# Kernel optimization log

Measured on AMD Instinct MI355X. Metric: run time of the kernel, lower is better.

Reference implementation:

```python
import jax, jax.numpy as jnp
import numpy as np

HID = 768
NUM_HEADS = 12
HEAD_DIM = HID // NUM_HEADS
MASK_VALUE = -1.0e9
EPS = 1.0e-4  # module's self.eps, also used as the diagonal fill constant


def setup_inputs() -> dict:
    key = jax.random.key(0)
    k1, k2, k3 = jax.random.split(key, 3)
    B, M = 16, 512
    ocr_features = jax.random.normal(k1, (B, M, HID), dtype=jnp.float32)
    # prior neighbor-attention from previous layer, probabilities in [0,1)
    prior = jax.random.uniform(k2, (B, 1, M, M), dtype=jnp.float32)
    Wq = jax.random.normal(k3, (HID, HID), dtype=jnp.float32) / np.sqrt(HID)
    bq = jnp.zeros((HID,), dtype=jnp.float32)
    ocr_features_mask = jnp.ones((B, M), dtype=jnp.int32)
    return {"ocr_features": ocr_features, "prior": prior, "Wq": Wq, "bq": bq,
            "ocr_features_mask": ocr_features_mask}


def reference(ocr_features, prior, Wq, bq, ocr_features_mask):
    B, M, _ = ocr_features.shape
    # Module uses q_linear for Q, K (and V, which is unused) -> Q == K.
    q = (ocr_features @ Wq + bq).reshape(B, M, NUM_HEADS, HEAD_DIM)
    q = q.transpose(0, 2, 1, 3)  # (B, H, M, D)
    # note: scaled by head_dim (not sqrt), as in the source
    scores = jnp.einsum('bhid,bhjd->bhij', q, q) / HEAD_DIM  # (B, H, M, M)

    dt = scores.dtype
    prev_word_mask = jnp.eye(M, k=1, dtype=dt)   # superdiagonal
    next_word_mask = jnp.eye(M, k=-1, dtype=dt)  # subdiagonal
    main_diag_mask = jnp.eye(M, dtype=dt)

    # neighbor mask: only prev/next word positions that are valid OCR tokens
    neibor_mask = ((prev_word_mask + next_word_mask)[None, :, :] > 0) & \
                  (ocr_features_mask[:, None, :] > 0)  # (B, M, M)
    scores = jnp.where(neibor_mask[:, None, :, :], scores, MASK_VALUE)
    neibor_attn = jax.nn.softmax(scores, axis=-1)
    # symmetrize: sqrt(a * a^T + eps)
    neibor_attn = jnp.sqrt(neibor_attn * jnp.swapaxes(neibor_attn, -1, -2) + EPS)
    neibor_attn = prior + (1.0 - prior) * neibor_attn

    # log-space cumulative product via triangular matmuls
    tri = jnp.triu(jnp.ones((M, M), dtype=dt))  # (M, M), incl. diagonal
    # keep only superdiagonal log-probs, cumulative-sum to the right via tri
    t = jnp.where(prev_word_mask > 0, jnp.log(neibor_attn + 1e-9), 0.0) @ tri
    g_attn = jnp.exp(jnp.einsum('ij,bhjk->bhik', tri, t))
    # zero out diagonal and lower triangle (tri - diag == 0 there)
    g_attn = jnp.where((tri - main_diag_mask) > 0, g_attn, 0.0)
    g_attn = g_attn + jnp.swapaxes(g_attn, -1, -2) + \
             jnp.where(main_diag_mask > 0, neibor_attn, EPS)
    return (g_attn, neibor_attn)
```

## Files before the change

kernel.cpp:

```cpp
#include <hip/hip_runtime.h>
#include <cstdint>
#include <cstddef>

#define B_   16
#define M_   512
#define HID_ 768
#define NH_  12
#define HD_  64

typedef short s16x8 __attribute__((ext_vector_type(8)));
typedef float f32x4 __attribute__((ext_vector_type(4)));
typedef unsigned short u16x8 __attribute__((ext_vector_type(8)));
typedef unsigned short u16x4 __attribute__((ext_vector_type(4)));

__device__ __forceinline__ unsigned short f2bf(float f) {
    unsigned int u = __builtin_bit_cast(unsigned int, f);
    u = u + 0x7FFFu + ((u >> 16) & 1u);
    return (unsigned short)(u >> 16);
}

__device__ __forceinline__ void gld_lds16(const void* g, void* lds) {
    __builtin_amdgcn_global_load_lds(
        (const __attribute__((address_space(1))) unsigned int*)g,
        (__attribute__((address_space(3))) unsigned int*)lds,
        16, 0, 0);
}

__device__ __forceinline__ int csx(int r, int c) {
    return (r << 7) | (c ^ (r & 31));
}

__launch_bounds__(256)
__global__ void prep(const float* __restrict__ X, const float* __restrict__ W,
                     unsigned short* __restrict__ Xb, unsigned short* __restrict__ Wt) {
    __shared__ float T[32][33];
    const int blk = blockIdx.x;
    const int t   = threadIdx.x;
    if (blk < 3072) {
        const size_t i = ((size_t)blk * 256 + t) * 8;
        const float4 a = *(const float4*)(X + i);
        const float4 b = *(const float4*)(X + i + 4);
        u16x8 v = { f2bf(a.x), f2bf(a.y), f2bf(a.z), f2bf(a.w),
                    f2bf(b.x), f2bf(b.y), f2bf(b.z), f2bf(b.w) };
        *(u16x8*)(Xb + i) = v;
    } else {
        const int tb = blk - 3072;
        const int n0 = (tb % 24) * 32;
        const int k0 = (tb / 24) * 32;
        #pragma unroll
        for (int p = 0; p < 4; ++p) {
            const int r = p * 8 + (t >> 5);
            const int c = t & 31;
            T[r][c] = W[(size_t)(k0 + r) * HID_ + n0 + c];
        }
        __syncthreads();
        const int nl = t >> 3;
        const int k4 = (t & 7) * 4;
        u16x4 v = { f2bf(T[k4 + 0][nl]), f2bf(T[k4 + 1][nl]),
                    f2bf(T[k4 + 2][nl]), f2bf(T[k4 + 3][nl]) };
        *(u16x4*)(Wt + (size_t)(n0 + nl) * HID_ + k0 + k4) = v;
    }
}

__launch_bounds__(256)
__global__ void gemm_dots(const unsigned short* __restrict__ Xb,
                          const unsigned short* __restrict__ Wt,
                          const float* __restrict__ bq,
                          float* __restrict__ sdot, float* __restrict__ Qedge) {
    __shared__ float smem[64 * 128];
    __shared__ float partial[128];
    unsigned short* As = (unsigned short*)smem;
    unsigned short* Bs = (unsigned short*)smem + 64 * 64;
    float* Cs = smem;

    const int tid  = threadIdx.x;
    const int lane = tid & 63;
    const int wave = tid >> 6;
    const int wr   = (wave >> 1) * 32;
    const int wc   = (wave & 1) * 64;
    const int ln   = lane & 15;
    const int quad = lane >> 4;

    const int bid = blockIdx.x;
    const int li  = bid >> 3;
    const int by  = ((bid & 7) << 4) + li / 6;
    const int bx  = li % 6;
    const int r0  = by * 64;
    const int n0  = bx * 128;

    const int srow  = lane >> 3;
    const int selem = ((lane & 7) ^ (lane >> 3)) * 8;
    const int swz   = (ln & 7) << 4;

    f32x4 acc[2][4] = {};

    for (int kt = 0; kt < HID_ / 64; ++kt) {
        const int k0 = kt * 64;
        #pragma unroll
        for (int c = wave * 2; c < wave * 2 + 2; ++c) {
            const unsigned short* ga = Xb + (size_t)(r0 + c * 8 + srow) * HID_ + k0 + selem;
            gld_lds16(ga, (char*)As + c * 1024);
        }
        #pragma unroll
        for (int c = wave * 4; c < wave * 4 + 4; ++c) {
            const unsigned short* gb = Wt + (size_t)(n0 + c * 8 + srow) * HID_ + k0 + selem;
            gld_lds16(gb, (char*)Bs + c * 1024);
        }
        __syncthreads();

        #pragma unroll
        for (int kk = 0; kk < 2; ++kk) {
            s16x8 af[2], bf[4];
            #pragma unroll
            for (int r = 0; r < 2; ++r)
                af[r] = *(const s16x8*)((const char*)As + (wr + r * 16 + ln) * 128
                                        + ((kk * 64 + quad * 16) ^ swz));
            #pragma unroll
            for (int c = 0; c < 4; ++c)
                bf[c] = *(const s16x8*)((const char*)Bs + (wc + c * 16 + ln) * 128
                                        + ((kk * 64 + quad * 16) ^ swz));
            #pragma unroll
            for (int r = 0; r < 2; ++r)
                #pragma unroll
                for (int c = 0; c < 4; ++c)
                    acc[r][c] = __builtin_amdgcn_mfma_f32_16x16x32_bf16(af[r], bf[c], acc[r][c], 0, 0, 0);
        }
        __syncthreads();
    }

    #pragma unroll
    for (int c = 0; c < 4; ++c) {
        const int col = wc + c * 16 + ln;
        const float bias = bq[n0 + col];
        #pragma unroll
        for (int r = 0; r < 2; ++r) {
            const int rowb = wr + r * 16 + quad * 4;
            #pragma unroll
            for (int e = 0; e < 4; ++e)
                Cs[csx(rowb + e, col)] = acc[r][c][e] + bias;
        }
    }
    __syncthreads();

    {
        const int s   = tid >> 7;
        const int col = tid & 127;
        const int row = s ? 63 : 0;
        Qedge[(size_t)(by * 2 + s) * HID_ + n0 + col] = Cs[csx(row, col)];
    }

    {
        const int p  = tid & 63;
        const int hh = (tid >> 6) & 1;
        const int dh = tid >> 7;
        float s0 = 0.f, s1 = 0.f;
        if (p < 63) {
            const int base = hh * 64 + dh * 32;
            #pragma unroll
            for (int d = 0; d < 32; d += 2) {
                s0 += Cs[csx(p, base + d)]     * Cs[csx(p + 1, base + d)];
                s1 += Cs[csx(p, base + d + 1)] * Cs[csx(p + 1, base + d + 1)];
            }
        }
        if (dh) partial[(hh << 6) | p] = s0 + s1;
        __syncthreads();
        if (!dh && p < 63) {
            const float tot = s0 + s1 + partial[(hh << 6) | p];
            const int g  = by * 64 + p;
            const int bb = g >> 9;
            const int ii = g & 511;
            const int h  = bx * 2 + hh;
            sdot[(size_t)(bb * NH_ + h) * M_ + ii] = tot * (1.f / 64.f);
        }
    }
}

__launch_bounds__(512)
__global__ void scanstats(const float* __restrict__ sdot, const float* __restrict__ Qedge,
                          const float* __restrict__ prior, const int* __restrict__ mask,
                          float* __restrict__ na_super, float* __restrict__ na_sub,
                          float* __restrict__ Ssum) {
    const int bh = blockIdx.x;
    const int b  = bh / NH_;
    const int h  = bh - b * NH_;
    const int i  = threadIdx.x;
    const int lane = i & 63;
    const int wid  = i >> 6;

    __shared__ float sh_s[M_];
    __shared__ float sh_pp[M_];
    __shared__ float wsum[8];

    float s = 0.f;
    if (i < M_ - 1) {
        if ((i & 63) == 63) {
            const int gby = (b << 3) + (i >> 6);
            const float* qa = Qedge + (size_t)(gby * 2 + 1) * HID_ + h * HD_;
            const float* qb = Qedge + (size_t)(gby + 1) * 2 * HID_ + h * HD_;
            float a0 = 0.f, a1 = 0.f;
            #pragma unroll
            for (int d = 0; d < HD_; d += 8) {
                const float4 xa = *(const float4*)(qa + d);
                const float4 xb = *(const float4*)(qb + d);
                const float4 ya = *(const float4*)(qa + d + 4);
                const float4 yb = *(const float4*)(qb + d + 4);
                a0 += xa.x * xb.x + xa.y * xb.y + xa.z * xb.z + xa.w * xb.w;
                a1 += ya.x * yb.x + ya.y * yb.y + ya.z * yb.z + ya.w * yb.w;
            }
            s = (a0 + a1) * (1.f / 64.f);
        } else {
            s = sdot[bh * M_ + i];
        }
    }
    sh_s[i] = s;
    __syncthreads();

    const bool vp = (i > 0)      && (mask[b * M_ + i - 1] > 0);
    const bool vn = (i < M_ - 1) && (mask[b * M_ + i + 1] > 0);
    const float sp = vp ? sh_s[i - 1] : -1e30f;
    const float sn = vn ? s : -1e30f;
    const float mx = fmaxf(sp, sn);
    const float ep = vp ? __expf(sp - mx) : 0.f;
    const float en = vn ? __expf(sn - mx) : 0.f;
    float den = ep + en;
    den = (den > 0.f) ? den : 1.f;
    const float pp = ep / den;
    const float pn = en / den;
    sh_pp[i] = pp;
    __syncthreads();

    float Lv = 0.f;
    if (i < M_ - 1) {
        const float  sym = sqrtf(pn * sh_pp[i + 1] + 1e-4f);
        const size_t pb  = (size_t)b * (M_ * M_);
        const float  prs = prior[pb + (size_t)i * M_ + (i + 1)];
        const float  prb = prior[pb + (size_t)(i + 1) * M_ + i];
        const float  nsup = prs + (1.f - prs) * sym;
        na_super[bh * M_ + i] = nsup;
        na_sub[bh * M_ + i]   = prb + (1.f - prb) * sym;
        Lv = logf(nsup + 1e-9f);
    }

    float v = Lv;
    #pragma unroll
    for (int off = 1; off < 64; off <<= 1) {
        float tt = __shfl_up(v, off, 64);
        if (lane >= off) v += tt;
    }
    if (lane == 63) wsum[wid] = v;
    __syncthreads();
    float base = 0.f;
    for (int w = 0; w < wid; ++w) base += wsum[w];
    Ssum[bh * M_ + i] = v + base - Lv;
}

__launch_bounds__(256)
__global__ void fill_out(const float* __restrict__ prior,
                         const float* __restrict__ na_super,
                         const float* __restrict__ na_sub,
                         const float* __restrict__ Ssum,
                         float* __restrict__ out) {
    const int tid = threadIdx.x;
    const int bi  = blockIdx.x;
    const int b   = bi >> 8;
    const int i   = ((bi & 255) << 1) | (tid >> 7);
    const int j0  = (tid & 127) * 4;

    const f32x4 pr4 = __builtin_nontemporal_load(
        (const f32x4*)(prior + (size_t)b * (M_ * M_) + (size_t)i * M_ + j0));
    const float pv[4] = {pr4[0], pr4[1], pr4[2], pr4[3]};
    const float c0 = 0.00999999977f;
    const size_t half = (size_t)B_ * NH_ * M_ * M_;

    #pragma unroll 2
    for (int h = 0; h < NH_; ++h) {
        const int bh = b * NH_ + h;
        const float4 S4 = *(const float4*)(Ssum + (size_t)bh * M_ + j0);
        const float  Si = Ssum[bh * M_ + i];
        const float  nsup_i   = (i < M_ - 1) ? na_super[bh * M_ + i]   : 0.f;
        const float  nsub_im1 = (i > 0)      ? na_sub[bh * M_ + i - 1] : 0.f;
        const float sv[4] = {S4.x, S4.y, S4.z, S4.w};

        f32x4 nav, ggv;
        #pragma unroll
        for (int e = 0; e < 4; ++e) {
            const int j = j0 + e;
            float na = fmaf(pv[e], 1.f - c0, c0);
            if (j == i - 1) na = nsub_im1;
            if (j == i + 1) na = nsup_i;
            const float d = sv[e] - Si;
            float g = __expf((j > i) ? d : -d) + 1e-4f;
            if (j == i) g = na;
            nav[e] = na;
            ggv[e] = g;
        }

        const size_t off = ((size_t)(bh * M_ + i)) * M_ + j0;
        __builtin_nontemporal_store(ggv, (f32x4*)(out + off));
        __builtin_nontemporal_store(nav, (f32x4*)(out + half + off));
    }
}

extern "C" void kernel_launch(void* const* d_in, const int* in_sizes, int n_in,
                              void* d_out, int out_size, void* d_ws, size_t ws_size,
                              hipStream_t stream) {
    const float* X     = (const float*)d_in[0];
    const float* prior = (const float*)d_in[1];
    const float* Wq    = (const float*)d_in[2];
    const float* bq    = (const float*)d_in[3];
    const int*   msk   = (const int*)  d_in[4];
    float* out = (float*)d_out;

    float* na_super = (float*)d_ws;
    float* na_sub   = na_super + (size_t)B_ * NH_ * M_;
    float* Ssum     = na_sub   + (size_t)B_ * NH_ * M_;
    float* sdot     = Ssum     + (size_t)B_ * NH_ * M_;
    float* Qedge    = sdot     + (size_t)B_ * NH_ * M_;
    unsigned short* Xb = (unsigned short*)(Qedge + (size_t)128 * 2 * HID_);
    unsigned short* Wt = Xb + (size_t)B_ * M_ * HID_;

    prep<<<3072 + 576, 256, 0, stream>>>(X, Wq, Xb, Wt);

    gemm_dots<<<768, 256, 0, stream>>>(Xb, Wt, bq, sdot, Qedge);

    scanstats<<<B_ * NH_, M_, 0, stream>>>(sdot, Qedge, prior, msk, na_super, na_sub, Ssum);

    fill_out<<<B_ * (M_ / 2), 256, 0, stream>>>(prior, na_super, na_sub, Ssum, out);
}
```

Baseline: 453.7 us.

## Move bulk neighbor-attention output writes into GEMM kernel to overlap with MFMA

The bulk of the neighbor-attention output (prior*(1-c0)+c0 for every head) is now written from inside the GEMM kernel's k-loop, spread across iterations, so those memory stores overlap with matrix compute. The scan kernel scatters the sub- and superdiagonal values straight into the output, and fill_out writes only the g_attn half plus the diagonal. This removes the na_super/na_sub workspace and halves the store traffic in the last kernel. In exchange the GEMM gains extra global traffic that may compete with its tile loads, and correctness now depends on the order of the three kernels' writes.

```diff
diff --git a/kernel.cpp b/kernel.cpp
--- a/kernel.cpp
+++ b/kernel.cpp
@@ -12,6 +12,8 @@
 typedef float f32x4 __attribute__((ext_vector_type(4)));
 typedef unsigned short u16x8 __attribute__((ext_vector_type(8)));
 typedef unsigned short u16x4 __attribute__((ext_vector_type(4)));
+
+#define C0_ 0.00999999977f
 
 __device__ __forceinline__ unsigned short f2bf(float f) {
     unsigned int u = __builtin_bit_cast(unsigned int, f);
@@ -66,7 +68,9 @@
 __global__ void gemm_dots(const unsigned short* __restrict__ Xb,
                           const unsigned short* __restrict__ Wt,
                           const float* __restrict__ bq,
-                          float* __restrict__ sdot, float* __restrict__ Qedge) {
+                          const float* __restrict__ prior,
+                          float* __restrict__ sdot, float* __restrict__ Qedge,
+                          float* __restrict__ out) {
     __shared__ float smem[64 * 128];
     __shared__ float partial[128];
     unsigned short* As = (unsigned short*)smem;
@@ -92,6 +96,9 @@
     const int selem = ((lane & 7) ^ (lane >> 3)) * 8;
     const int swz   = (ln & 7) << 4;
 
+    const size_t half  = (size_t)B_ * NH_ * M_ * M_;
+    const int    fbase = bid * 65536 + tid * 4;
+
     f32x4 acc[2][4] = {};
 
     for (int kt = 0; kt < HID_ / 64; ++kt) {
@@ -107,6 +114,24 @@
             gld_lds16(gb, (char*)Bs + c * 1024);
         }
         __syncthreads();
+
+        {
+            const int qb = kt * 6;
+            #pragma unroll
+            for (int qq = 0; qq < 6; ++qq) {
+                const int q = qb + qq;
+                if (q < 64) {
+                    const int f   = fbase + (q << 10);
+                    const int bh  = f >> 18;
+                    const int bb2 = bh / NH_;
+                    const int rem = f & 0x3FFFF;
+                    const float4 p4 = *(const float4*)(prior + ((size_t)bb2 << 18) + rem);
+                    f32x4 na4 = { fmaf(p4.x, 1.f - C0_, C0_), fmaf(p4.y, 1.f - C0_, C0_),
+                                  fmaf(p4.z, 1.f - C0_, C0_), fmaf(p4.w, 1.f - C0_, C0_) };
+                    __builtin_nontemporal_store(na4, (f32x4*)(out + half + f));
+                }
+            }
+        }
 
         #pragma unroll
         for (int kk = 0; kk < 2; ++kk) {
@@ -178,8 +203,7 @@
 __launch_bounds__(512)
 __global__ void scanstats(const float* __restrict__ sdot, const float* __restrict__ Qedge,
                           const float* __restrict__ prior, const int* __restrict__ mask,
-                          float* __restrict__ na_super, float* __restrict__ na_sub,
-                          float* __restrict__ Ssum) {
+                          float* __restrict__ Ssum, float* __restrict__ out) {
     const int bh = blockIdx.x;
     const int b  = bh / NH_;
     const int h  = bh - b * NH_;
@@ -236,9 +260,12 @@
         const float  prs = prior[pb + (size_t)i * M_ + (i + 1)];
         const float  prb = prior[pb + (size_t)(i + 1) * M_ + i];
         const float  nsup = prs + (1.f - prs) * sym;
-        na_super[bh * M_ + i] = nsup;
-        na_sub[bh * M_ + i]   = prb + (1.f - prb) * sym;
+        const float  nsub = prb + (1.f - prb) * sym;
         Lv = logf(nsup + 1e-9f);
+        const size_t half = (size_t)B_ * NH_ * M_ * M_;
+        const size_t nab  = half + (size_t)bh * (M_ * M_);
+        out[nab + (size_t)i * M_ + (i + 1)] = nsup;
+        out[nab + (size_t)(i + 1) * M_ + i] = nsub;
     }
 
     float v = Lv;
@@ -256,8 +283,6 @@
 
 __launch_bounds__(256)
 __global__ void fill_out(const float* __restrict__ prior,
-                         const float* __restrict__ na_super,
-                         const float* __restrict__ na_sub,
                          const float* __restrict__ Ssum,
                          float* __restrict__ out) {
     const int tid = threadIdx.x;
@@ -266,38 +291,28 @@
     const int i   = ((bi & 255) << 1) | (tid >> 7);
     const int j0  = (tid & 127) * 4;
 
-    const f32x4 pr4 = __builtin_nontemporal_load(
-        (const f32x4*)(prior + (size_t)b * (M_ * M_) + (size_t)i * M_ + j0));
-    const float pv[4] = {pr4[0], pr4[1], pr4[2], pr4[3]};
-    const float c0 = 0.00999999977f;
-    const size_t half = (size_t)B_ * NH_ * M_ * M_;
+    const float prd = prior[(size_t)b * (M_ * M_) + (size_t)i * (M_ + 1)];
+    const float nad = fmaf(prd, 1.f - C0_, C0_);
 
     #pragma unroll 2
     for (int h = 0; h < NH_; ++h) {
         const int bh = b * NH_ + h;
         const float4 S4 = *(const float4*)(Ssum + (size_t)bh * M_ + j0);
         const float  Si = Ssum[bh * M_ + i];
-        const float  nsup_i   = (i < M_ - 1) ? na_super[bh * M_ + i]   : 0.f;
-        const float  nsub_im1 = (i > 0)      ? na_sub[bh * M_ + i - 1] : 0.f;
         const float sv[4] = {S4.x, S4.y, S4.z, S4.w};
 
-        f32x4 nav, ggv;
+        f32x4 ggv;
         #pragma unroll
         for (int e = 0; e < 4; ++e) {
             const int j = j0 + e;
-            float na = fmaf(pv[e], 1.f - c0, c0);
-            if (j == i - 1) na = nsub_im1;
-            if (j == i + 1) na = nsup_i;
             const float d = sv[e] - Si;
             float g = __expf((j > i) ? d : -d) + 1e-4f;
-            if (j == i) g = na;
-            nav[e] = na;
+            if (j == i) g = nad;
             ggv[e] = g;
         }
 
         const size_t off = ((size_t)(bh * M_ + i)) * M_ + j0;
         __builtin_nontemporal_store(ggv, (f32x4*)(out + off));
-        __builtin_nontemporal_store(nav, (f32x4*)(out + half + off));
     }
 }
 
@@ -311,19 +326,17 @@
     const int*   msk   = (const int*)  d_in[4];
     float* out = (float*)d_out;
 
-    float* na_super = (float*)d_ws;
-    float* na_sub   = na_super + (size_t)B_ * NH_ * M_;
-    float* Ssum     = na_sub   + (size_t)B_ * NH_ * M_;
-    float* sdot     = Ssum     + (size_t)B_ * NH_ * M_;
-    float* Qedge    = sdot     + (size_t)B_ * NH_ * M_;
+    float* Ssum  = (float*)d_ws;
+    float* sdot  = Ssum + (size_t)B_ * NH_ * M_;
+    float* Qedge = sdot + (size_t)B_ * NH_ * M_;
     unsigned short* Xb = (unsigned short*)(Qedge + (size_t)128 * 2 * HID_);
     unsigned short* Wt = Xb + (size_t)B_ * M_ * HID_;
 
     prep<<<3072 + 576, 256, 0, stream>>>(X, Wq, Xb, Wt);
 
-    gemm_dots<<<768, 256, 0, stream>>>(Xb, Wt, bq, sdot, Qedge);
-
-    scanstats<<<B_ * NH_, M_, 0, stream>>>(sdot, Qedge, prior, msk, na_super, na_sub, Ssum);
-
-    fill_out<<<B_ * (M_ / 2), 256, 0, stream>>>(prior, na_super, na_sub, Ssum, out);
-}
+    gemm_dots<<<768, 256, 0, stream>>>(Xb, Wt, bq, prior, sdot, Qedge, out);
+
+    scanstats<<<B_ * NH_, M_, 0, stream>>>(sdot, Qedge, prior, msk, Ssum, out);
+
+    fill_out<<<B_ * (M_ / 2), 256, 0, stream>>>(prior, Ssum, out);
+}
```

After: 470.9 us. 3.8% more time.
